# Optimization experiments

Measured on AMD Instinct MI355X. Metric: run time of the kernel, lower is better.

## Reference

```python
import jax, jax.numpy as jnp
import numpy as np

D = 256
B, S, N = 4, 512, 4


def setup_inputs() -> dict:
    key = jax.random.key(0)
    ks = jax.random.split(key, 24)
    d, dq = D, D // 4
    std = 0.02
    inp = {
        'x':   jax.random.normal(ks[0], (B, S, N, d), jnp.float32),
        'Wq':  jax.random.normal(ks[1], (d, d), jnp.float32) * std,
        'Wk':  jax.random.normal(ks[2], (d, d), jnp.float32) * std,
        'Wv':  jax.random.normal(ks[3], (d, d), jnp.float32) * std,
        'Wg1': jax.random.normal(ks[4], (d, d), jnp.float32) * std,
        'bg1': jnp.zeros((d,), jnp.float32),
        'Wg2': jax.random.normal(ks[5], (d, d), jnp.float32) * std,
        'bg2': jnp.zeros((d,), jnp.float32),
        'We1': jax.random.normal(ks[6], (d, dq), jnp.float32) * std,
        'be1': jnp.zeros((dq,), jnp.float32),
        'We2': jax.random.normal(ks[7], (dq, 1), jnp.float32) * std,
        'be2': jnp.zeros((1,), jnp.float32),
        'Wa1': jax.random.normal(ks[8], (d, dq), jnp.float32) * std,
        'ba1': jnp.zeros((dq,), jnp.float32),
        'Wa2': jax.random.normal(ks[9], (dq, 1), jnp.float32) * std,
        'ba2': jnp.zeros((1,), jnp.float32),
        'Wo':  jax.random.normal(ks[10], (d, d), jnp.float32) * std,
        'bo':  jnp.zeros((d,), jnp.float32),
        'gamma': jnp.ones((d,), jnp.float32),
        'beta':  jnp.zeros((d,), jnp.float32),
    }
    return inp


def reference(x, Wq, Wk, Wv, Wg1, bg1, Wg2, bg2, We1, be1, We2, be2,
              Wa1, ba1, Wa2, ba2, Wo, bo, gamma, beta):
    b, s, n, f = x.shape
    xf = x.reshape(b * n, s, f)  # matches torch .view on contiguous x
    residual = xf

    q = xf @ Wq                                    # [bn, s, d]
    k = xf @ Wk
    v = xf @ Wv
    v_hat = jax.nn.silu(v @ Wg1 + bg1) @ Wg2 + bg2  # value_generator
    eta = jax.nn.sigmoid(jax.nn.silu(xf @ We1 + be1) @ We2 + be2) * 0.1 + 0.01   # [bn, s, 1]
    alpha = jax.nn.sigmoid(jax.nn.silu(xf @ Wa1 + ba1) @ Wa2 + ba2) * 0.5 + 0.5  # [bn, s, 1]

    # F.normalize(k, dim=-1): eps = 1e-12
    kn = k / jnp.maximum(jnp.linalg.norm(k, axis=-1, keepdims=True), 1e-12)

    M0 = jnp.zeros((b * n, f, f), x.dtype)

    def step(M, inp):
        q_t, k_t, v_t, e_t, a_t = inp  # [bn,d],[bn,d],[bn,d],[bn,1],[bn,1]
        out_t = jnp.einsum('bij,bj->bi', M, q_t)
        Mk = jnp.einsum('bij,bj->bi', M, k_t)
        e = e_t[:, :, None]  # [bn,1,1]
        a = a_t[:, :, None]
        # delta rule: M <- a*M - e*(Mk k^T) + e*(v k^T)
        M_new = a * M + e * ((v_t - Mk)[:, :, None] * k_t[:, None, :])
        return M_new, out_t

    seq = (jnp.swapaxes(q, 0, 1), jnp.swapaxes(kn, 0, 1), jnp.swapaxes(v_hat, 0, 1),
           jnp.swapaxes(eta, 0, 1), jnp.swapaxes(alpha, 0, 1))
    M, outs = jax.lax.scan(step, M0, seq)
    out = jnp.swapaxes(outs, 0, 1)  # [bn, s, d]

    y = out @ Wo + bo + residual  # dropout is identity in eval/reference
    mu = jnp.mean(y, axis=-1, keepdims=True)
    var = jnp.var(y, axis=-1, keepdims=True)
    y = (y - mu) / jnp.sqrt(var + 1e-5) * gamma + beta
    return y.reshape(b, s, n, f), M
```

## Files before the change

### kernel.cpp

```cpp
#include <hip/hip_runtime.h>

#define F_ 256
#define S_ 512
#define NH_ 16
#define CCH 32
#define NCH (S_/CCH)
#define KSTR 264
#define TSTR 40

typedef __attribute__((ext_vector_type(8))) short short8_t;
typedef __attribute__((ext_vector_type(4))) float f32x4;

#define BARX() do { \
  asm volatile("s_waitcnt lgkmcnt(0)" ::: "memory"); \
  __builtin_amdgcn_s_barrier(); \
  __builtin_amdgcn_sched_barrier(0); \
} while (0)

__device__ __forceinline__ float sigmoid_f(float x) { return 1.0f / (1.0f + __expf(-x)); }

__device__ __forceinline__ ushort f2bf(float x) {
  uint u = __float_as_uint(x);
  u += 0x7FFFu + ((u >> 16) & 1u);
  return (ushort)(u >> 16);
}
__device__ __forceinline__ float bf2f(ushort u) {
  return __uint_as_float((uint)u << 16);
}

template<int CTRL>
__device__ __forceinline__ float dpp_add(float x) {
  int y = __builtin_amdgcn_update_dpp(0, __float_as_int(x), CTRL, 0xf, 0xf, true);
  return x + __int_as_float(y);
}
__device__ __forceinline__ float red8(float x) {
  x = dpp_add<0xB1>(x);
  x = dpp_add<0x4E>(x);
  x = dpp_add<0x141>(x);
  return x;
}

__global__ __launch_bounds__(256) void wconv_k(
    const float* __restrict__ Wq, const float* __restrict__ Wk,
    const float* __restrict__ Wv, const float* __restrict__ Wg1,
    const float* __restrict__ Wg2, const float* __restrict__ Wo,
    const float* __restrict__ We1, const float* __restrict__ Wa1,
    const float* __restrict__ be1, const float* __restrict__ ba1,
    ushort* __restrict__ Wt, float* __restrict__ beas)
{
  const int blk = blockIdx.x, tid = threadIdx.x;
  if (blk == 104) {
    if (tid < 64) beas[tid] = be1[tid];
    else if (tid < 128) beas[tid] = ba1[tid - 64];
    return;
  }
  __shared__ float tile[64][65];
  const float* src; int N, k0, n0; size_t dstbase;
  if (blk < 96) {
    const int w = blk >> 4, tl = blk & 15;
    const float* ws_[6] = {Wq, Wk, Wv, Wg1, Wg2, Wo};
    const size_t dstb[6] = {0, 65536, 131072, 229376, 294912, 360448};
    src = ws_[w]; N = 256;
    k0 = (tl >> 2) * 64; n0 = (tl & 3) * 64;
    dstbase = dstb[w];
  } else {
    const int w = (blk - 96) >> 2, tl = (blk - 96) & 3;
    src = w ? Wa1 : We1; N = 64;
    k0 = tl * 64; n0 = 0;
    dstbase = w ? 212992 : 196608;
  }
  #pragma unroll
  for (int p = 0; p < 4; ++p) {
    const int idx = (p << 8) + tid;
    const int r = idx >> 4, c4 = (idx & 15) << 2;
    if (c4 < N) {
      const float4 v = *(const float4*)&src[(size_t)(k0 + r) * N + n0 + c4];
      tile[r][c4 + 0] = v.x; tile[r][c4 + 1] = v.y;
      tile[r][c4 + 2] = v.z; tile[r][c4 + 3] = v.w;
    }
  }
  __syncthreads();
  #pragma unroll
  for (int p = 0; p < 4; ++p) {
    const int idx = (p << 8) + tid;
    const int nl = idx >> 4, kc = (idx & 15) << 2;
    if ((n0 + nl) < ((blk < 96) ? 256 : 64)) {
      ushort4 o;
      o.x = f2bf(tile[kc + 0][nl]); o.y = f2bf(tile[kc + 1][nl]);
      o.z = f2bf(tile[kc + 2][nl]); o.w = f2bf(tile[kc + 3][nl]);
      *(ushort4*)&Wt[dstbase + (size_t)(n0 + nl) * 256 + k0 + kc] = o;
    }
  }
}

__global__ __launch_bounds__(256) void qkve_k(
    const float* __restrict__ x, const ushort* __restrict__ Wt,
    const float* __restrict__ beas,
    ushort* __restrict__ qb, float* __restrict__ kf,
    ushort* __restrict__ vb, float* __restrict__ sesa)
{
  __shared__ ushort As[2][64 * 72];
  __shared__ ushort Ws[2][64 * 72];
  const int tid = threadIdx.x;
  const int wv = tid >> 6, l = tid & 63;
  const int ln = l & 15, hi = l >> 4, hi4 = hi << 2, hi8 = hi << 3;
  const int wr = wv >> 1, wc = wv & 1;
  const int row0 = blockIdx.y * 64, col0 = blockIdx.x * 64;
  const int r_ = tid >> 3, c8_ = (tid & 7) << 3;

  float4 pAf[4];
  short8_t pB[2];
  auto loadT = [&](int k0) {
    pAf[0] = *(const float4*)&x[(size_t)(row0 + r_) * 256 + k0 + c8_];
    pAf[1] = *(const float4*)&x[(size_t)(row0 + r_) * 256 + k0 + c8_ + 4];
    pAf[2] = *(const float4*)&x[(size_t)(row0 + 32 + r_) * 256 + k0 + c8_];
    pAf[3] = *(const float4*)&x[(size_t)(row0 + 32 + r_) * 256 + k0 + c8_ + 4];
    pB[0] = *(const short8_t*)&Wt[(size_t)(col0 + r_) * 256 + k0 + c8_];
    pB[1] = *(const short8_t*)&Wt[(size_t)(col0 + 32 + r_) * 256 + k0 + c8_];
  };
  auto commitT = [&](int b) {
    #pragma unroll
    for (int h = 0; h < 2; ++h) {
      short8_t s;
      s[0] = (short)f2bf(pAf[h*2].x); s[1] = (short)f2bf(pAf[h*2].y);
      s[2] = (short)f2bf(pAf[h*2].z); s[3] = (short)f2bf(pAf[h*2].w);
      s[4] = (short)f2bf(pAf[h*2+1].x); s[5] = (short)f2bf(pAf[h*2+1].y);
      s[6] = (short)f2bf(pAf[h*2+1].z); s[7] = (short)f2bf(pAf[h*2+1].w);
      *(short8_t*)&As[b][(h * 32 + r_) * 72 + c8_] = s;
    }
    *(short8_t*)&Ws[b][r_ * 72 + c8_] = pB[0];
    *(short8_t*)&Ws[b][(32 + r_) * 72 + c8_] = pB[1];
  };

  f32x4 acc[2][2];
  #pragma unroll
  for (int i = 0; i < 2; ++i)
    #pragma unroll
    for (int j = 0; j < 2; ++j)
      #pragma unroll
      for (int r = 0; r < 4; ++r) acc[i][j][r] = 0.f;

  loadT(0); commitT(0); __syncthreads();
  #pragma unroll
  for (int t = 0; t < 4; ++t) {
    const int b = t & 1;
    if (t < 3) loadT((t + 1) << 6);
    #pragma unroll
    for (int kk = 0; kk < 2; ++kk) {
      short8_t a0 = *(const short8_t*)&As[b][(wr * 32 + ln) * 72 + kk * 32 + hi8];
      short8_t a1 = *(const short8_t*)&As[b][(wr * 32 + 16 + ln) * 72 + kk * 32 + hi8];
      short8_t b0 = *(const short8_t*)&Ws[b][(wc * 32 + ln) * 72 + kk * 32 + hi8];
      short8_t b1 = *(const short8_t*)&Ws[b][(wc * 32 + 16 + ln) * 72 + kk * 32 + hi8];
      acc[0][0] = __builtin_amdgcn_mfma_f32_16x16x32_bf16(a0, b0, acc[0][0], 0, 0, 0);
      acc[0][1] = __builtin_amdgcn_mfma_f32_16x16x32_bf16(a0, b1, acc[0][1], 0, 0, 0);
      acc[1][0] = __builtin_amdgcn_mfma_f32_16x16x32_bf16(a1, b0, acc[1][0], 0, 0, 0);
      acc[1][1] = __builtin_amdgcn_mfma_f32_16x16x32_bf16(a1, b1, acc[1][1], 0, 0, 0);
    }
    if (t < 3) commitT(b ^ 1);
    __syncthreads();
  }

  #pragma unroll
  for (int mi = 0; mi < 2; ++mi)
    #pragma unroll
    for (int ni = 0; ni < 2; ++ni) {
      const int col = col0 + wc * 32 + ni * 16 + ln;
      #pragma unroll
      for (int r = 0; r < 4; ++r) {
        const int row = row0 + wr * 32 + mi * 16 + hi4 + r;
        float vx = acc[mi][ni][r];
        if (col0 < 256)      qb[(size_t)row * 256 + col] = f2bf(vx);
        else if (col0 < 512) kf[(size_t)row * 256 + (col - 256)] = vx;
        else if (col0 < 768) vb[(size_t)row * 256 + (col - 512)] = f2bf(vx);
        else {
          const int cc = col - 768;
          vx += beas[cc];
          vx *= sigmoid_f(vx);
          sesa[(size_t)row * 128 + cc] = vx;
        }
      }
    }
}

__global__ __launch_bounds__(256) void gemm_bf16_k(
    const ushort* __restrict__ A, const ushort* __restrict__ Wt,
    const float* __restrict__ bias, float* __restrict__ Cf,
    ushort* __restrict__ Cb, int act)
{
  __shared__ ushort As[2][64 * 72];
  __shared__ ushort Ws[2][64 * 72];
  const int tid = threadIdx.x;
  const int wv = tid >> 6, l = tid & 63;
  const int ln = l & 15, hi = l >> 4, hi4 = hi << 2, hi8 = hi << 3;
  const int wr = wv >> 1, wc = wv & 1;
  const int row0 = blockIdx.y * 64, col0 = blockIdx.x * 64;
  const int r_ = tid >> 3, c8_ = (tid & 7) << 3;

  short8_t pA[2], pB[2];
  auto loadT = [&](int k0) {
    pA[0] = *(const short8_t*)&A[(size_t)(row0 + r_) * 256 + k0 + c8_];
    pA[1] = *(const short8_t*)&A[(size_t)(row0 + 32 + r_) * 256 + k0 + c8_];
    pB[0] = *(const short8_t*)&Wt[(size_t)(col0 + r_) * 256 + k0 + c8_];
    pB[1] = *(const short8_t*)&Wt[(size_t)(col0 + 32 + r_) * 256 + k0 + c8_];
  };
  auto commitT = [&](int b) {
    *(short8_t*)&As[b][r_ * 72 + c8_] = pA[0];
    *(short8_t*)&As[b][(32 + r_) * 72 + c8_] = pA[1];
    *(short8_t*)&Ws[b][r_ * 72 + c8_] = pB[0];
    *(short8_t*)&Ws[b][(32 + r_) * 72 + c8_] = pB[1];
  };

  f32x4 acc[2][2];
  #pragma unroll
  for (int i = 0; i < 2; ++i)
    #pragma unroll
    for (int j = 0; j < 2; ++j)
      #pragma unroll
      for (int r = 0; r < 4; ++r) acc[i][j][r] = 0.f;

  loadT(0); commitT(0); __syncthreads();
  #pragma unroll
  for (int t = 0; t < 4; ++t) {
    const int b = t & 1;
    if (t < 3) loadT((t + 1) << 6);
    #pragma unroll
    for (int kk = 0; kk < 2; ++kk) {
      short8_t a0 = *(const short8_t*)&As[b][(wr * 32 + ln) * 72 + kk * 32 + hi8];
      short8_t a1 = *(const short8_t*)&As[b][(wr * 32 + 16 + ln) * 72 + kk * 32 + hi8];
      short8_t b0 = *(const short8_t*)&Ws[b][(wc * 32 + ln) * 72 + kk * 32 + hi8];
      short8_t b1 = *(const short8_t*)&Ws[b][(wc * 32 + 16 + ln) * 72 + kk * 32 + hi8];
      acc[0][0] = __builtin_amdgcn_mfma_f32_16x16x32_bf16(a0, b0, acc[0][0], 0, 0, 0);
      acc[0][1] = __builtin_amdgcn_mfma_f32_16x16x32_bf16(a0, b1, acc[0][1], 0, 0, 0);
      acc[1][0] = __builtin_amdgcn_mfma_f32_16x16x32_bf16(a1, b0, acc[1][0], 0, 0, 0);
      acc[1][1] = __builtin_amdgcn_mfma_f32_16x16x32_bf16(a1, b1, acc[1][1], 0, 0, 0);
    }
    if (t < 3) commitT(b ^ 1);
    __syncthreads();
  }

  #pragma unroll
  for (int mi = 0; mi < 2; ++mi)
    #pragma unroll
    for (int ni = 0; ni < 2; ++ni) {
      const int col = col0 + wc * 32 + ni * 16 + ln;
      const float bval = bias ? bias[col] : 0.f;
      #pragma unroll
      for (int r = 0; r < 4; ++r) {
        const int row = row0 + wr * 32 + mi * 16 + hi4 + r;
        float vx = acc[mi][ni][r] + bval;
        if (act == 1) vx = vx * sigmoid_f(vx);
        if (Cf) Cf[(size_t)row * 256 + col] = vx;
        if (Cb) Cb[(size_t)row * 256 + col] = f2bf(vx);
      }
    }
}

__global__ __launch_bounds__(256) void g1prep_k(
    const ushort* __restrict__ vb, const ushort* __restrict__ WtG1,
    const float* __restrict__ bg1, ushort* __restrict__ t1b,
    const ushort* __restrict__ kb, const ushort* __restrict__ qb,
    const float* __restrict__ eta, const float* __restrict__ alpha,
    ushort* __restrict__ Tg, ushort* __restrict__ Gqg, float* __restrict__ Sg,
    ushort* __restrict__ Ktg)
{
  __shared__ __align__(16) char smem[38592];
  const int blk = blockIdx.x;
  const int tid = threadIdx.x;
  const int l = tid & 63, wv = tid >> 6;
  const int ln = l & 15, hi = l >> 4, hi4 = hi << 2, hi8 = hi << 3;

  if (blk < 512) {
    ushort* As = (ushort*)smem;
    ushort* Ws = (ushort*)(smem + 18432);
    const int wr = wv >> 1, wc = wv & 1;
    const int row0 = (blk >> 2) * 64, col0 = (blk & 3) * 64;
    const int r_ = tid >> 3, c8_ = (tid & 7) << 3;

    short8_t pA[2], pB[2];
    auto loadT = [&](int k0) {
      pA[0] = *(const short8_t*)&vb[(size_t)(row0 + r_) * 256 + k0 + c8_];
      pA[1] = *(const short8_t*)&vb[(size_t)(row0 + 32 + r_) * 256 + k0 + c8_];
      pB[0] = *(const short8_t*)&WtG1[(size_t)(col0 + r_) * 256 + k0 + c8_];
      pB[1] = *(const short8_t*)&WtG1[(size_t)(col0 + 32 + r_) * 256 + k0 + c8_];
    };
    auto commitT = [&](int b) {
      *(short8_t*)&As[b * 4608 + r_ * 72 + c8_] = pA[0];
      *(short8_t*)&As[b * 4608 + (32 + r_) * 72 + c8_] = pA[1];
      *(short8_t*)&Ws[b * 4608 + r_ * 72 + c8_] = pB[0];
      *(short8_t*)&Ws[b * 4608 + (32 + r_) * 72 + c8_] = pB[1];
    };

    f32x4 acc[2][2];
    #pragma unroll
    for (int i = 0; i < 2; ++i)
      #pragma unroll
      for (int j = 0; j < 2; ++j)
        #pragma unroll
        for (int r = 0; r < 4; ++r) acc[i][j][r] = 0.f;

    loadT(0); commitT(0); __syncthreads();
    #pragma unroll
    for (int t = 0; t < 4; ++t) {
      const int b = t & 1;
      if (t < 3) loadT((t + 1) << 6);
      #pragma unroll
      for (int kk = 0; kk < 2; ++kk) {
        short8_t a0 = *(const short8_t*)&As[b * 4608 + (wr * 32 + ln) * 72 + kk * 32 + hi8];
        short8_t a1 = *(const short8_t*)&As[b * 4608 + (wr * 32 + 16 + ln) * 72 + kk * 32 + hi8];
        short8_t b0 = *(const short8_t*)&Ws[b * 4608 + (wc * 32 + ln) * 72 + kk * 32 + hi8];
        short8_t b1 = *(const short8_t*)&Ws[b * 4608 + (wc * 32 + 16 + ln) * 72 + kk * 32 + hi8];
        acc[0][0] = __builtin_amdgcn_mfma_f32_16x16x32_bf16(a0, b0, acc[0][0], 0, 0, 0);
        acc[0][1] = __builtin_amdgcn_mfma_f32_16x16x32_bf16(a0, b1, acc[0][1], 0, 0, 0);
        acc[1][0] = __builtin_amdgcn_mfma_f32_16x16x32_bf16(a1, b0, acc[1][0], 0, 0, 0);
        acc[1][1] = __builtin_amdgcn_mfma_f32_16x16x32_bf16(a1, b1, acc[1][1], 0, 0, 0);
      }
      if (t < 3) commitT(b ^ 1);
      __syncthreads();
    }

    #pragma unroll
    for (int mi = 0; mi < 2; ++mi)
      #pragma unroll
      for (int ni = 0; ni < 2; ++ni) {
        const int col = col0 + wc * 32 + ni * 16 + ln;
        const float bval = bg1[col];
        #pragma unroll
        for (int r = 0; r < 4; ++r) {
          const int row = row0 + wr * 32 + mi * 16 + hi4 + r;
          float vx = acc[mi][ni][r] + bval;
          vx = vx * sigmoid_f(vx);
          t1b[(size_t)row * 256 + col] = f2bf(vx);
        }
      }
    return;
  }

  const int pb = blk - 512;
  const int ch = pb & 15, h = pb >> 4;
  const int t0 = ch * CCH;
  ushort* K_lds = (ushort*)smem;
  ushort* Q_lds = (ushort*)(smem + 16896);
  float*  G_lds = (float*)(smem + 33792);
  float*  ea    = (float*)(smem + 37888);
  float*  scal  = (float*)(smem + 38144);

  const ushort* kg = kb + (size_t)(h * S_ + t0) * F_;
  const ushort* qg = qb + (size_t)(h * S_ + t0) * F_;
  #pragma unroll
  for (int w = 0; w < 4; ++w) {
    int o = w * 256 + tid; int t = o >> 5, c8 = (o & 31) << 3;
    *(short8_t*)&K_lds[t * KSTR + c8] = *(const short8_t*)&kg[(size_t)t * F_ + c8];
    *(short8_t*)&Q_lds[t * KSTR + c8] = *(const short8_t*)&qg[(size_t)t * F_ + c8];
  }
  if (tid < CCH)            ea[tid] = eta[(size_t)h * S_ + t0 + tid];
  else if (tid < 2 * CCH)   ea[tid] = alpha[(size_t)h * S_ + t0 + tid - CCH];
  __syncthreads();

  {
    const int tt = tid & 31, cl = tid >> 5;
    for (int cp = 0; cp < 32; ++cp) {
      const int c = cp * 8 + cl;
      Ktg[((size_t)h * F_ + c) * S_ + t0 + tt] = K_lds[tt * KSTR + c];
    }
  }

  {
    const int tI = wv >> 1, tJ = wv & 1;
    f32x4 accG = {0.f, 0.f, 0.f, 0.f};
    f32x4 accQ = {0.f, 0.f, 0.f, 0.f};
    #pragma unroll
    for (int ko = 0; ko < 8; ++ko) {
      const int cb = ko * 32 + hi8;
      short8_t bfr = *(const short8_t*)&K_lds[(tJ * 16 + ln) * KSTR + cb];
      short8_t aK  = *(const short8_t*)&K_lds[(tI * 16 + ln) * KSTR + cb];
      short8_t aQ  = *(const short8_t*)&Q_lds[(tI * 16 + ln) * KSTR + cb];
      accG = __builtin_amdgcn_mfma_f32_16x16x32_bf16(aK, bfr, accG, 0, 0, 0);
      accQ = __builtin_amdgcn_mfma_f32_16x16x32_bf16(aQ, bfr, accQ, 0, 0, 0);
    }
    ushort* Gqo = Gqg + (size_t)(h * NCH + ch) * (CCH * CCH);
    #pragma unroll
    for (int r = 0; r < 4; ++r) {
      const int t = tI * 16 + hi4 + r, s = tJ * 16 + ln;
      G_lds[t * CCH + s] = accG[r];
      Gqo[t * CCH + s] = (s < t) ? f2bf(accQ[r]) : (ushort)0;
    }
  }
  if (tid == 0) {
    float gp = 1.f;
    for (int t = 0; t < CCH; ++t) {
      const float a = ea[CCH + t], e = ea[t];
      const float gm = gp * a;
      scal[t]           = e / a;
      scal[CCH + t]     = e / gm;
      scal[2 * CCH + t] = gp;
      gp = gm;
    }
    scal[3 * CCH] = gp;
  }
  __syncthreads();

  {
    const int j = tid >> 3, g = tid & 7;
    float x0 = 0.f, x1 = 0.f, x2 = 0.f, x3 = 0.f;
    ushort* To = Tg + (size_t)(h * NCH + ch) * (CCH * CCH);
    #pragma unroll
    for (int t = 0; t < CCH; ++t) {
      float p = 0.f;
      const f32x4 gr = *(const f32x4*)&G_lds[t * CCH + 4 * g];
      if (4 * g + 0 < t) p += gr[0] * x0;
      if (4 * g + 1 < t) p += gr[1] * x1;
      if (4 * g + 2 < t) p += gr[2] * x2;
      if (4 * g + 3 < t) p += gr[3] * x3;
      const float tot = red8(p);
      const float xt = ((t == j) ? 1.f : 0.f) - scal[t] * tot;
      if (g == (t >> 2)) {
        if ((t & 3) == 0) x0 = xt; else if ((t & 3) == 1) x1 = xt;
        else if ((t & 3) == 2) x2 = xt; else x3 = xt;
      }
      if (g == 0) To[t * CCH + j] = f2bf(xt);
    }
  }
  if (tid < 97) Sg[(size_t)(h * NCH + ch) * 128 + tid] = scal[tid];
}

__global__ __launch_bounds__(256) void gemmo_ln_k(
    const ushort* __restrict__ A, const ushort* __restrict__ Wt,
    const float* __restrict__ bo, const float* __restrict__ x,
    const float* __restrict__ gamma, const float* __restrict__ beta,
    float* __restrict__ y)
{
  __shared__ ushort As[2][32 * 72];
  __shared__ ushort Ws[2][256 * 72];
  __shared__ float rs_[2][32];
  __shared__ float rq_[2][32];
  const int tid = threadIdx.x;
  const int wv = tid >> 6, l = tid & 63;
  const int ln = l & 15, hi = l >> 4, hi4 = hi << 2, hi8 = hi << 3;
  const int g = wv >> 1, chf = wv & 1;
  const int row0 = blockIdx.x * 32;

  short8_t pA, pW[8];
  auto loadT = [&](int k0) {
    { const int r = tid >> 3, c8 = (tid & 7) << 3;
      pA = *(const short8_t*)&A[(size_t)(row0 + r) * 256 + k0 + c8]; }
    #pragma unroll
    for (int p = 0; p < 8; ++p) {
      const int idx = (p << 8) + tid;
      const int n = idx >> 3, c8 = (idx & 7) << 3;
      pW[p] = *(const short8_t*)&Wt[(size_t)n * 256 + k0 + c8];
    }
  };
  auto commitT = [&](int b) {
    { const int r = tid >> 3, c8 = (tid & 7) << 3;
      *(short8_t*)&As[b][r * 72 + c8] = pA; }
    #pragma unroll
    for (int p = 0; p < 8; ++p) {
      const int idx = (p << 8) + tid;
      const int n = idx >> 3, c8 = (idx & 7) << 3;
      *(short8_t*)&Ws[b][n * 72 + c8] = pW[p];
    }
  };

  f32x4 acc[8];
  #pragma unroll
  for (int nt = 0; nt < 8; ++nt)
    #pragma unroll
    for (int r = 0; r < 4; ++r) acc[nt][r] = 0.f;

  loadT(0); commitT(0); __syncthreads();
  #pragma unroll
  for (int t = 0; t < 4; ++t) {
    const int b = t & 1;
    if (t < 3) loadT((t + 1) << 6);
    #pragma unroll
    for (int kk = 0; kk < 2; ++kk) {
      short8_t a = *(const short8_t*)&As[b][(g * 16 + ln) * 72 + kk * 32 + hi8];
      #pragma unroll
      for (int nt = 0; nt < 8; ++nt) {
        short8_t bb = *(const short8_t*)&Ws[b][(chf * 128 + nt * 16 + ln) * 72 + kk * 32 + hi8];
        acc[nt] = __builtin_amdgcn_mfma_f32_16x16x32_bf16(a, bb, acc[nt], 0, 0, 0);
      }
    }
    if (t < 3) commitT(b ^ 1);
    __syncthreads();
  }

  float val[8][4];
  float sm[4] = {0.f, 0.f, 0.f, 0.f}, sq[4] = {0.f, 0.f, 0.f, 0.f};
  #pragma unroll
  for (int nt = 0; nt < 8; ++nt) {
    const int col = chf * 128 + nt * 16 + ln;
    const float bv = bo[col];
    #pragma unroll
    for (int r = 0; r < 4; ++r) {
      const int row = row0 + g * 16 + hi4 + r;
      const float v = acc[nt][r] + bv + x[(size_t)row * 256 + col];
      val[nt][r] = v;
      sm[r] += v;
      sq[r] += v * v;
    }
  }
  #pragma unroll
  for (int m = 1; m < 16; m <<= 1) {
    #pragma unroll
    for (int r = 0; r < 4; ++r) {
      sm[r] += __shfl_xor(sm[r], m, 64);
      sq[r] += __shfl_xor(sq[r], m, 64);
    }
  }
  if (ln == 0) {
    #pragma unroll
    for (int r = 0; r < 4; ++r) {
      rs_[chf][g * 16 + hi4 + r] = sm[r];
      rq_[chf][g * 16 + hi4 + r] = sq[r];
    }
  }
  __syncthreads();
  #pragma unroll
  for (int r = 0; r < 4; ++r) {
    const int lr = g * 16 + hi4 + r;
    const float tot = rs_[0][lr] + rs_[1][lr];
    const float tq  = rq_[0][lr] + rq_[1][lr];
    const float mu  = tot * (1.0f / 256.0f);
    const float var = tq * (1.0f / 256.0f) - mu * mu;
    const float rstd = rsqrtf(var + 1e-5f);
    #pragma unroll
    for (int nt = 0; nt < 8; ++nt) {
      const int col = chf * 128 + nt * 16 + ln;
      y[(size_t)(row0 + lr) * 256 + col] =
          (val[nt][r] - mu) * rstd * gamma[col] + beta[col];
    }
  }
}

__global__ __launch_bounds__(256) void knea_k(
    const float* __restrict__ kf, ushort* __restrict__ kb,
    const float* __restrict__ sesa,
    const float* __restrict__ We2, const float* __restrict__ be2,
    const float* __restrict__ Wa2, const float* __restrict__ ba2,
    float* __restrict__ eta, float* __restrict__ alpha)
{
  const int lane = threadIdx.x & 63;
  const size_t row = ((size_t)blockIdx.x << 2) + (threadIdx.x >> 6);
  {
    const size_t off = row * F_ + ((size_t)lane << 2);
    float4 v = *(const float4*)&kf[off];
    float ss = v.x * v.x + v.y * v.y + v.z * v.z + v.w * v.w;
    #pragma unroll
    for (int m = 1; m < 64; m <<= 1) ss += __shfl_xor(ss, m, 64);
    const float sc = 1.0f / fmaxf(sqrtf(ss), 1e-12f);
    ushort4 o;
    o.x = f2bf(v.x * sc); o.y = f2bf(v.y * sc);
    o.z = f2bf(v.z * sc); o.w = f2bf(v.w * sc);
    *(ushort4*)&kb[off] = o;
  }
  {
    float pe = sesa[row * 128 + lane] * We2[lane];
    float pa = sesa[row * 128 + 64 + lane] * Wa2[lane];
    #pragma unroll
    for (int m = 1; m < 64; m <<= 1) {
      pe += __shfl_xor(pe, m, 64);
      pa += __shfl_xor(pa, m, 64);
    }
    if (lane == 0) {
      eta[row]   = sigmoid_f(pe + be2[0]) * 0.1f + 0.01f;
      alpha[row] = sigmoid_f(pa + ba2[0]) * 0.5f + 0.5f;
    }
  }
}

__global__ __launch_bounds__(256, 1) void scan_chunk_k(
    const ushort* __restrict__ kb, const ushort* __restrict__ qb,
    const ushort* __restrict__ vhb, const ushort* __restrict__ Ktg,
    const ushort* __restrict__ Tg, const ushort* __restrict__ Gqg,
    const float* __restrict__ Sg,
    ushort* __restrict__ outb, float* __restrict__ Mout)
{
  __shared__ ushort M_lds[16 * KSTR];
  __shared__ ushort Wt_lds[16 * TSTR];
  __shared__ ushort R_lds[16 * TSTR];
  __shared__ float  QM_lds[CCH * 20];

  const int tid = threadIdx.x;
  const int flat = blockIdx.x;
  const int h = (flat & 7) + (((flat >> 3) >> 4) << 3);
  const int slice = (flat >> 3) & 15;
  const int r0 = slice * 16;
  const int wv = tid >> 6, l = tid & 63;
  const int ln = l & 15, hi = l >> 4, hi4 = hi << 2, hi8 = hi << 3;

  for (int u = tid; u < 16 * KSTR / 8; u += 256) {
    short8_t z = {0, 0, 0, 0, 0, 0, 0, 0};
    *(short8_t*)&M_lds[u * 8] = z;
  }
  f32x4 Mf[4];
  #pragma unroll
  for (int q = 0; q < 4; ++q)
    #pragma unroll
    for (int r = 0; r < 4; ++r) Mf[q][r] = 0.f;

  const ushort* kgh = kb + (size_t)h * S_ * F_;
  const ushort* qgh = qb + (size_t)h * S_ * F_;
  const ushort* kth = Ktg + (size_t)h * F_ * S_;
  const ushort* vgh = vhb + (size_t)h * S_ * F_;

  struct Frags {
    short8_t P[8];
    short8_t Kt[4];
    short8_t T, Gq;
    ushort   V[4];
    float    b[4], c[4], gp[4];
    float    gC;
  };
  Frags fA, fB;

  auto loadchunk = [&](int ch, Frags& f) {
    const int t0 = ch * CCH;
    if (wv < 2) {
      #pragma unroll
      for (int ko = 0; ko < 8; ++ko)
        f.P[ko] = *(const short8_t*)&kgh[(size_t)(t0 + wv * 16 + ln) * F_ + ko * 32 + hi8];
      const size_t tb = (size_t)(h * NCH + ch) * (CCH * CCH);
      f.T  = *(const short8_t*)&Tg [tb + (size_t)(wv * 16 + ln) * CCH + hi8];
      f.Gq = *(const short8_t*)&Gqg[tb + (size_t)(wv * 16 + ln) * CCH + hi8];
      const size_t sb = (size_t)(h * NCH + ch) * 128;
      #pragma unroll
      for (int r = 0; r < 4; ++r) {
        const int t = wv * 16 + hi4 + r;
        f.V[r]  = vgh[(size_t)(t0 + t) * F_ + r0 + ln];
        f.b[r]  = Sg[sb + t];
        f.c[r]  = Sg[sb + 32 + t];
        f.gp[r] = Sg[sb + 64 + t];
      }
    } else {
      #pragma unroll
      for (int ko = 0; ko < 8; ++ko)
        f.P[ko] = *(const short8_t*)&qgh[(size_t)(t0 + (wv - 2) * 16 + ln) * F_ + ko * 32 + hi8];
    }
    #pragma unroll
    for (int qq = 0; qq < 4; ++qq)
      f.Kt[qq] = *(const short8_t*)&kth[(size_t)((wv * 4 + qq) * 16 + ln) * S_ + t0 + hi8];
    f.gC = Sg[(size_t)(h * NCH + ch) * 128 + 96];
  };

  auto CHUNK = [&](int ch, const Frags& f) {
    const int t0 = ch * CCH;
    if (wv < 2) {
      f32x4 a0 = {0.f, 0.f, 0.f, 0.f}, a1 = {0.f, 0.f, 0.f, 0.f};
      #pragma unroll
      for (int ko = 0; ko < 4; ++ko) {
        short8_t b0 = *(const short8_t*)&M_lds[ln * KSTR + (2 * ko) * 32 + hi8];
        a0 = __builtin_amdgcn_mfma_f32_16x16x32_bf16(f.P[2 * ko], b0, a0, 0, 0, 0);
        short8_t b1 = *(const short8_t*)&M_lds[ln * KSTR + (2 * ko + 1) * 32 + hi8];
        a1 = __builtin_amdgcn_mfma_f32_16x16x32_bf16(f.P[2 * ko + 1], b1, a1, 0, 0, 0);
      }
      ushort4 rw;
      float rv[4];
      #pragma unroll
      for (int r = 0; r < 4; ++r) {
        const float s = a0[r] + a1[r];
        rv[r] = f.c[r] * bf2f(f.V[r]) - f.b[r] * s;
      }
      rw.x = f2bf(rv[0]); rw.y = f2bf(rv[1]); rw.z = f2bf(rv[2]); rw.w = f2bf(rv[3]);
      *(ushort4*)&R_lds[ln * TSTR + wv * 16 + hi4] = rw;
    } else {
      f32x4 a0 = {0.f, 0.f, 0.f, 0.f}, a1 = {0.f, 0.f, 0.f, 0.f};
      #pragma unroll
      for (int ko = 0; ko < 4; ++ko) {
        short8_t b0 = *(const short8_t*)&M_lds[ln * KSTR + (2 * ko) * 32 + hi8];
        a0 = __builtin_amdgcn_mfma_f32_16x16x32_bf16(f.P[2 * ko], b0, a0, 0, 0, 0);
        short8_t b1 = *(const short8_t*)&M_lds[ln * KSTR + (2 * ko + 1) * 32 + hi8];
        a1 = __builtin_amdgcn_mfma_f32_16x16x32_bf16(f.P[2 * ko + 1], b1, a1, 0, 0, 0);
      }
      #pragma unroll
      for (int r = 0; r < 4; ++r)
        QM_lds[((wv - 2) * 16 + hi4 + r) * 20 + ln] = a0[r] + a1[r];
    }
    BARX();

    if (wv < 2) {
      short8_t bfr = *(const short8_t*)&R_lds[ln * TSTR + hi8];
      f32x4 z = {0.f, 0.f, 0.f, 0.f};
      f32x4 d = __builtin_amdgcn_mfma_f32_16x16x32_bf16(f.T, bfr, z, 0, 0, 0);
      ushort4 wo;
      wo.x = f2bf(d[0]); wo.y = f2bf(d[1]); wo.z = f2bf(d[2]); wo.w = f2bf(d[3]);
      *(ushort4*)&Wt_lds[ln * TSTR + wv * 16 + hi4] = wo;
    }
    BARX();

    {
      short8_t aw = *(const short8_t*)&Wt_lds[ln * TSTR + hi8];
      #pragma unroll
      for (int qq = 0; qq < 4; ++qq) {
        const int jt = wv * 4 + qq;
        f32x4 d = __builtin_amdgcn_mfma_f32_16x16x32_bf16(aw, f.Kt[qq], Mf[qq], 0, 0, 0);
        #pragma unroll
        for (int r = 0; r < 4; ++r) {
          const float nv = f.gC * d[r];
          Mf[qq][r] = nv;
          M_lds[(hi4 + r) * KSTR + jt * 16 + ln] = f2bf(nv);
        }
      }
      if (wv < 2) {
        f32x4 z = {0.f, 0.f, 0.f, 0.f};
        f32x4 d = __builtin_amdgcn_mfma_f32_16x16x32_bf16(f.Gq, aw, z, 0, 0, 0);
        #pragma unroll
        for (int r = 0; r < 4; ++r) {
          const int t = wv * 16 + hi4 + r;
          outb[(size_t)(h * S_ + t0 + t) * F_ + r0 + ln] =
              f2bf(f.gp[r] * (QM_lds[t * 20 + ln] + d[r]));
        }
      }
    }
    BARX();
  };

  loadchunk(0, fA);
  BARX();

  for (int ch = 0; ch < NCH; ch += 2) {
    loadchunk(ch + 1, fB);
    CHUNK(ch, fA);
    if (ch + 2 < NCH) loadchunk(ch + 2, fA);
    CHUNK(ch + 1, fB);
  }

  #pragma unroll
  for (int qq = 0; qq < 4; ++qq) {
    const int jt = wv * 4 + qq;
    #pragma unroll
    for (int r = 0; r < 4; ++r)
      Mout[((size_t)h * F_ + r0 + hi4 + r) * F_ + jt * 16 + ln] = Mf[qq][r];
  }
}

extern "C" void kernel_launch(void* const* d_in, const int* in_sizes, int n_in,
                              void* d_out, int out_size, void* d_ws, size_t ws_size,
                              hipStream_t stream)
{
  const float* x    = (const float*)d_in[0];
  const float* Wq   = (const float*)d_in[1];
  const float* Wk   = (const float*)d_in[2];
  const float* Wv   = (const float*)d_in[3];
  const float* Wg1  = (const float*)d_in[4];
  const float* bg1  = (const float*)d_in[5];
  const float* Wg2  = (const float*)d_in[6];
  const float* bg2  = (const float*)d_in[7];
  const float* We1  = (const float*)d_in[8];
  const float* be1  = (const float*)d_in[9];
  const float* We2  = (const float*)d_in[10];
  const float* be2  = (const float*)d_in[11];
  const float* Wa1  = (const float*)d_in[12];
  const float* ba1  = (const float*)d_in[13];
  const float* Wa2  = (const float*)d_in[14];
  const float* ba2  = (const float*)d_in[15];
  const float* Wo   = (const float*)d_in[16];
  const float* bo   = (const float*)d_in[17];
  const float* gamma= (const float*)d_in[18];
  const float* beta = (const float*)d_in[19];

  const int Mrows = NH_ * S_;
  const size_t MM = 1048576;
  const size_t NTF = 2 * MM;

  float* ws = (float*)d_ws;
  ushort* outb = (ushort*)(ws + 0 * MM);
  ushort* qb   = (ushort*)(ws + 1 * MM);
  ushort* kb   = (ushort*)(ws + 2 * MM);
  float*  kf   = ws + 3 * MM;
  ushort* t1b  = (ushort*)(ws + 3 * MM);
  ushort* vhb  = (ushort*)(ws + 4 * MM);
  ushort* vb   = (ushort*)(ws + 5 * MM);
  float*  sesa = ws + 6 * MM;
  float*  eta  = ws + 7 * MM;
  float*  alpha= eta + Mrows;
  ushort* Tg   = (ushort*)(ws + 7 * MM + 16384);
  ushort* Gqg  = Tg + 262144;
  float*  Sg   = ws + 7 * MM + 16384 + 131072 + 131072;
  ushort* Ktg  = (ushort*)(Sg + 32768);
  ushort* Wt   = Ktg + 2097152;
  float*  beas = (float*)(Wt + 425984);

  dim3 blk(256);

  wconv_k<<<105, blk, 0, stream>>>(Wq, Wk, Wv, Wg1, Wg2, Wo, We1, Wa1,
                                   be1, ba1, Wt, beas);

  qkve_k<<<dim3(14, 128), blk, 0, stream>>>(x, Wt, beas, qb, kf, vb, sesa);

  knea_k<<<Mrows / 4, blk, 0, stream>>>(kf, kb, sesa, We2, be2, Wa2, ba2, eta, alpha);

  g1prep_k<<<768, blk, 0, stream>>>(vb, Wt + 229376, bg1, t1b,
                                    kb, qb, eta, alpha, Tg, Gqg, Sg, Ktg);

  gemm_bf16_k<<<dim3(4, 128), blk, 0, stream>>>(t1b, Wt + 294912, bg2, nullptr, vhb, 0);

  float* yout = (float*)d_out;
  float* Mfin = yout + NTF;
  scan_chunk_k<<<256, blk, 0, stream>>>(kb, qb, vhb, Ktg, Tg, Gqg, Sg, outb, Mfin);

  gemmo_ln_k<<<256, blk, 0, stream>>>(outb, Wt + 360448, bo, x, gamma, beta, yout);
}
```

Baseline: 100.4 us.

## Process two 16-row state slices per block in chunked scan kernel

Each scan block now handles 32 rows of the state matrix (two 16-row slices) instead of 16, halving the grid from 256 to 128 blocks. The per-chunk fragments loaded from global memory (K, Q, K^T, T, Gq and scalars) are reused across both slices, cutting redundant global loads and barrier count per unit of work. In exchange it doubles register and LDS use per block, lengthens each block's serial work, and leaves only 128 blocks on a GPU with more CUs than that, which lowers parallelism.

```diff
diff --git a/kernel.cpp b/kernel.cpp
--- a/kernel.cpp
+++ b/kernel.cpp
@@ -576,28 +576,33 @@
     const float* __restrict__ Sg,
     ushort* __restrict__ outb, float* __restrict__ Mout)
 {
-  __shared__ ushort M_lds[16 * KSTR];
-  __shared__ ushort Wt_lds[16 * TSTR];
-  __shared__ ushort R_lds[16 * TSTR];
-  __shared__ float  QM_lds[CCH * 20];
+  __shared__ ushort M_lds[2][16 * KSTR];
+  __shared__ ushort Wt_lds[2][16 * TSTR];
+  __shared__ ushort R_lds[2][16 * TSTR];
+  __shared__ float  QM_lds[2][CCH * 20];
 
   const int tid = threadIdx.x;
   const int flat = blockIdx.x;
-  const int h = (flat & 7) + (((flat >> 3) >> 4) << 3);
-  const int slice = (flat >> 3) & 15;
-  const int r0 = slice * 16;
+  const int h = (flat & 7) + ((flat >> 6) << 3);
+  const int sp = (flat >> 3) & 7;
+  const int r0 = sp * 32;
   const int wv = tid >> 6, l = tid & 63;
   const int ln = l & 15, hi = l >> 4, hi4 = hi << 2, hi8 = hi << 3;
 
-  for (int u = tid; u < 16 * KSTR / 8; u += 256) {
-    short8_t z = {0, 0, 0, 0, 0, 0, 0, 0};
-    *(short8_t*)&M_lds[u * 8] = z;
-  }
-  f32x4 Mf[4];
-  #pragma unroll
-  for (int q = 0; q < 4; ++q)
-    #pragma unroll
-    for (int r = 0; r < 4; ++r) Mf[q][r] = 0.f;
+  {
+    ushort* mb = &M_lds[0][0];
+    for (int u = tid; u < 2 * 16 * KSTR / 8; u += 256) {
+      short8_t z = {0, 0, 0, 0, 0, 0, 0, 0};
+      *(short8_t*)&mb[u * 8] = z;
+    }
+  }
+  f32x4 Mf[2][4];
+  #pragma unroll
+  for (int cn = 0; cn < 2; ++cn)
+    #pragma unroll
+    for (int q = 0; q < 4; ++q)
+      #pragma unroll
+      for (int r = 0; r < 4; ++r) Mf[cn][q][r] = 0.f;
 
   const ushort* kgh = kb + (size_t)h * S_ * F_;
   const ushort* qgh = qb + (size_t)h * S_ * F_;
@@ -608,7 +613,7 @@
     short8_t P[8];
     short8_t Kt[4];
     short8_t T, Gq;
-    ushort   V[4];
+    ushort   V[2][4];
     float    b[4], c[4], gp[4];
     float    gC;
   };
@@ -627,7 +632,8 @@
       #pragma unroll
       for (int r = 0; r < 4; ++r) {
         const int t = wv * 16 + hi4 + r;
-        f.V[r]  = vgh[(size_t)(t0 + t) * F_ + r0 + ln];
+        f.V[0][r] = vgh[(size_t)(t0 + t) * F_ + r0 + ln];
+        f.V[1][r] = vgh[(size_t)(t0 + t) * F_ + r0 + 16 + ln];
         f.b[r]  = Sg[sb + t];
         f.c[r]  = Sg[sb + 32 + t];
         f.gp[r] = Sg[sb + 64 + t];
@@ -646,59 +652,69 @@
   auto CHUNK = [&](int ch, const Frags& f) {
     const int t0 = ch * CCH;
     if (wv < 2) {
-      f32x4 a0 = {0.f, 0.f, 0.f, 0.f}, a1 = {0.f, 0.f, 0.f, 0.f};
-      #pragma unroll
-      for (int ko = 0; ko < 4; ++ko) {
-        short8_t b0 = *(const short8_t*)&M_lds[ln * KSTR + (2 * ko) * 32 + hi8];
-        a0 = __builtin_amdgcn_mfma_f32_16x16x32_bf16(f.P[2 * ko], b0, a0, 0, 0, 0);
-        short8_t b1 = *(const short8_t*)&M_lds[ln * KSTR + (2 * ko + 1) * 32 + hi8];
-        a1 = __builtin_amdgcn_mfma_f32_16x16x32_bf16(f.P[2 * ko + 1], b1, a1, 0, 0, 0);
-      }
-      ushort4 rw;
-      float rv[4];
-      #pragma unroll
-      for (int r = 0; r < 4; ++r) {
-        const float s = a0[r] + a1[r];
-        rv[r] = f.c[r] * bf2f(f.V[r]) - f.b[r] * s;
-      }
-      rw.x = f2bf(rv[0]); rw.y = f2bf(rv[1]); rw.z = f2bf(rv[2]); rw.w = f2bf(rv[3]);
-      *(ushort4*)&R_lds[ln * TSTR + wv * 16 + hi4] = rw;
+      #pragma unroll
+      for (int cn = 0; cn < 2; ++cn) {
+        f32x4 a0 = {0.f, 0.f, 0.f, 0.f}, a1 = {0.f, 0.f, 0.f, 0.f};
+        #pragma unroll
+        for (int ko = 0; ko < 4; ++ko) {
+          short8_t b0 = *(const short8_t*)&M_lds[cn][ln * KSTR + (2 * ko) * 32 + hi8];
+          a0 = __builtin_amdgcn_mfma_f32_16x16x32_bf16(f.P[2 * ko], b0, a0, 0, 0, 0);
+          short8_t b1 = *(const short8_t*)&M_lds[cn][ln * KSTR + (2 * ko + 1) * 32 + hi8];
+          a1 = __builtin_amdgcn_mfma_f32_16x16x32_bf16(f.P[2 * ko + 1], b1, a1, 0, 0, 0);
+        }
+        ushort4 rw;
+        float rv[4];
+        #pragma unroll
+        for (int r = 0; r < 4; ++r) {
+          const float s = a0[r] + a1[r];
+          rv[r] = f.c[r] * bf2f(f.V[cn][r]) - f.b[r] * s;
+        }
+        rw.x = f2bf(rv[0]); rw.y = f2bf(rv[1]); rw.z = f2bf(rv[2]); rw.w = f2bf(rv[3]);
+        *(ushort4*)&R_lds[cn][ln * TSTR + wv * 16 + hi4] = rw;
+      }
     } else {
-      f32x4 a0 = {0.f, 0.f, 0.f, 0.f}, a1 = {0.f, 0.f, 0.f, 0.f};
-      #pragma unroll
-      for (int ko = 0; ko < 4; ++ko) {
-        short8_t b0 = *(const short8_t*)&M_lds[ln * KSTR + (2 * ko) * 32 + hi8];
-        a0 = __builtin_amdgcn_mfma_f32_16x16x32_bf16(f.P[2 * ko], b0, a0, 0, 0, 0);
-        short8_t b1 = *(const short8_t*)&M_lds[ln * KSTR + (2 * ko + 1) * 32 + hi8];
-        a1 = __builtin_amdgcn_mfma_f32_16x16x32_bf16(f.P[2 * ko + 1], b1, a1, 0, 0, 0);
-      }
-      #pragma unroll
-      for (int r = 0; r < 4; ++r)
-        QM_lds[((wv - 2) * 16 + hi4 + r) * 20 + ln] = a0[r] + a1[r];
+      #pragma unroll
+      for (int cn = 0; cn < 2; ++cn) {
+        f32x4 a0 = {0.f, 0.f, 0.f, 0.f}, a1 = {0.f, 0.f, 0.f, 0.f};
+        #pragma unroll
+        for (int ko = 0; ko < 4; ++ko) {
+          short8_t b0 = *(const short8_t*)&M_lds[cn][ln * KSTR + (2 * ko) * 32 + hi8];
+          a0 = __builtin_amdgcn_mfma_f32_16x16x32_bf16(f.P[2 * ko], b0, a0, 0, 0, 0);
+          short8_t b1 = *(const short8_t*)&M_lds[cn][ln * KSTR + (2 * ko + 1) * 32 + hi8];
+          a1 = __builtin_amdgcn_mfma_f32_16x16x32_bf16(f.P[2 * ko + 1], b1, a1, 0, 0, 0);
+        }
+        #pragma unroll
+        for (int r = 0; r < 4; ++r)
+          QM_lds[cn][((wv - 2) * 16 + hi4 + r) * 20 + ln] = a0[r] + a1[r];
+      }
     }
     BARX();
 
     if (wv < 2) {
-      short8_t bfr = *(const short8_t*)&R_lds[ln * TSTR + hi8];
-      f32x4 z = {0.f, 0.f, 0.f, 0.f};
-      f32x4 d = __builtin_amdgcn_mfma_f32_16x16x32_bf16(f.T, bfr, z, 0, 0, 0);
-      ushort4 wo;
-      wo.x = f2bf(d[0]); wo.y = f2bf(d[1]); wo.z = f2bf(d[2]); wo.w = f2bf(d[3]);
-      *(ushort4*)&Wt_lds[ln * TSTR + wv * 16 + hi4] = wo;
+      #pragma unroll
+      for (int cn = 0; cn < 2; ++cn) {
+        short8_t bfr = *(const short8_t*)&R_lds[cn][ln * TSTR + hi8];
+        f32x4 z = {0.f, 0.f, 0.f, 0.f};
+        f32x4 d = __builtin_amdgcn_mfma_f32_16x16x32_bf16(f.T, bfr, z, 0, 0, 0);
+        ushort4 wo;
+        wo.x = f2bf(d[0]); wo.y = f2bf(d[1]); wo.z = f2bf(d[2]); wo.w = f2bf(d[3]);
+        *(ushort4*)&Wt_lds[cn][ln * TSTR + wv * 16 + hi4] = wo;
+      }
     }
     BARX();
 
-    {
-      short8_t aw = *(const short8_t*)&Wt_lds[ln * TSTR + hi8];
+    #pragma unroll
+    for (int cn = 0; cn < 2; ++cn) {
+      short8_t aw = *(const short8_t*)&Wt_lds[cn][ln * TSTR + hi8];
       #pragma unroll
       for (int qq = 0; qq < 4; ++qq) {
         const int jt = wv * 4 + qq;
-        f32x4 d = __builtin_amdgcn_mfma_f32_16x16x32_bf16(aw, f.Kt[qq], Mf[qq], 0, 0, 0);
+        f32x4 d = __builtin_amdgcn_mfma_f32_16x16x32_bf16(aw, f.Kt[qq], Mf[cn][qq], 0, 0, 0);
         #pragma unroll
         for (int r = 0; r < 4; ++r) {
           const float nv = f.gC * d[r];
-          Mf[qq][r] = nv;
-          M_lds[(hi4 + r) * KSTR + jt * 16 + ln] = f2bf(nv);
+          Mf[cn][qq][r] = nv;
+          M_lds[cn][(hi4 + r) * KSTR + jt * 16 + ln] = f2bf(nv);
         }
       }
       if (wv < 2) {
@@ -707,8 +723,8 @@
         #pragma unroll
         for (int r = 0; r < 4; ++r) {
           const int t = wv * 16 + hi4 + r;
-          outb[(size_t)(h * S_ + t0 + t) * F_ + r0 + ln] =
-              f2bf(f.gp[r] * (QM_lds[t * 20 + ln] + d[r]));
+          outb[(size_t)(h * S_ + t0 + t) * F_ + r0 + cn * 16 + ln] =
+              f2bf(f.gp[r] * (QM_lds[cn][t * 20 + ln] + d[r]));
         }
       }
     }
@@ -726,12 +742,14 @@
   }
 
   #pragma unroll
-  for (int qq = 0; qq < 4; ++qq) {
-    const int jt = wv * 4 + qq;
-    #pragma unroll
-    for (int r = 0; r < 4; ++r)
-      Mout[((size_t)h * F_ + r0 + hi4 + r) * F_ + jt * 16 + ln] = Mf[qq][r];
-  }
+  for (int cn = 0; cn < 2; ++cn)
+    #pragma unroll
+    for (int qq = 0; qq < 4; ++qq) {
+      const int jt = wv * 4 + qq;
+      #pragma unroll
+      for (int r = 0; r < 4; ++r)
+        Mout[((size_t)h * F_ + r0 + cn * 16 + hi4 + r) * F_ + jt * 16 + ln] = Mf[cn][qq][r];
+    }
 }
 
 extern "C" void kernel_launch(void* const* d_in, const int* in_sizes, int n_in,
@@ -797,7 +815,7 @@
 
   float* yout = (float*)d_out;
   float* Mfin = yout + NTF;
-  scan_chunk_k<<<256, blk, 0, stream>>>(kb, qb, vhb, Ktg, Tg, Gqg, Sg, outb, Mfin);
+  scan_chunk_k<<<128, blk, 0, stream>>>(kb, qb, vhb, Ktg, Tg, Gqg, Sg, outb, Mfin);
 
   gemmo_ln_k<<<256, blk, 0, stream>>>(outb, Wt + 360448, bo, x, gamma, beta, yout);
 }
```

Measured after the change: 111.3 us. 1.11x slower.
